# Optimization experiments

Hardware: AMD Instinct MI355X
Metric: run time of the kernel (lower is better)

Reference implementation:

```python
import jax, jax.numpy as jnp
import numpy as np
import math

NUM_HEADS = 16
HEAD_DIM = 64
EMBED = 1024
NUM_BUCKETS = 32
MAX_DISTANCE = 128


def _relative_position_bucket(relative_position, num_buckets=NUM_BUCKETS, max_distance=MAX_DISTANCE):
    # bidirectional T5 bucketing
    nb = num_buckets // 2
    relative_buckets = (relative_position > 0).astype(jnp.int32) * nb
    rp = jnp.abs(relative_position)
    max_exact = nb // 2
    is_small = rp < max_exact
    rp_safe = jnp.maximum(rp, 1)  # avoid log(0); masked by is_small anyway
    rp_large = max_exact + (
        jnp.log(rp_safe.astype(jnp.float32) / max_exact)
        / math.log(max_distance / max_exact)
        * (nb - max_exact)
    ).astype(jnp.int32)
    rp_large = jnp.minimum(rp_large, nb - 1)
    return relative_buckets + jnp.where(is_small, rp, rp_large)


def compute_bias(rel_emb, q_len, k_len):
    ctx = jnp.arange(q_len)[:, None]
    mem = jnp.arange(k_len)[None, :]
    buckets = _relative_position_bucket(mem - ctx)  # [q,k]
    values = rel_emb[buckets]                       # [q,k,H]
    return jnp.transpose(values, (2, 0, 1))[None]   # [1,H,q,k]


def setup_inputs() -> dict:
    key = jax.random.key(0)
    ks = jax.random.split(key, 6)
    std = 0.02
    B, S = 2, 2048
    inner = NUM_HEADS * HEAD_DIM
    return {
        "input_ids": jax.random.normal(ks[0], (B, S, EMBED), dtype=jnp.float32),
        "Wq": jax.random.normal(ks[1], (EMBED, inner), dtype=jnp.float32) * std,
        "Wk": jax.random.normal(ks[2], (EMBED, inner), dtype=jnp.float32) * std,
        "Wv": jax.random.normal(ks[3], (EMBED, inner), dtype=jnp.float32) * std,
        "Wo": jax.random.normal(ks[4], (inner, EMBED), dtype=jnp.float32) * std,
        "rel_emb": jax.random.normal(ks[5], (NUM_BUCKETS, NUM_HEADS), dtype=jnp.float32) * std,
    }


def reference(input_ids, Wq, Wk, Wv, Wo, rel_emb):
    B, S, _ = input_ids.shape
    H, D = NUM_HEADS, HEAD_DIM
    q = (input_ids @ Wq).reshape(B, S, H, D).transpose(0, 2, 1, 3)  # [B,H,S,D]
    k = (input_ids @ Wk).reshape(B, S, H, D).transpose(0, 2, 1, 3)
    v = (input_ids @ Wv).reshape(B, S, H, D).transpose(0, 2, 1, 3)
    scores = jnp.einsum("bhqd,bhkd->bhqk", q, k)  # no 1/sqrt(d) scaling (T5 style)
    position_bias = compute_bias(rel_emb, S, S)   # [1,H,S,S]
    scores = scores + position_bias
    attn = jax.nn.softmax(scores, axis=-1)
    out = jnp.einsum("bhqk,bhkd->bhqd", attn, v)
    out = out.transpose(0, 2, 1, 3).reshape(B, S, H * D)
    out = out @ Wo
    return out, position_bias
```

## Files before the change

### kernel.cpp

```cpp
#include <hip/hip_runtime.h>
#include <stdint.h>

#define S_LEN 2048
#define NH 16
#define EMB 1024
#define L2E 1.44269504f

typedef __attribute__((ext_vector_type(8))) short bf16x8;
typedef __attribute__((ext_vector_type(4))) float floatx4;
typedef const __attribute__((address_space(1))) unsigned int* gas_u32p;
typedef __attribute__((address_space(3))) unsigned int* las_u32p;

static __device__ __forceinline__ void gld_lds16(const void* g, void* l) {
  __builtin_amdgcn_global_load_lds((gas_u32p)g, (las_u32p)l, 16, 0, 0);
}

static __device__ __forceinline__ unsigned short f2bf(float f) {
  unsigned int u = __float_as_uint(f);
  unsigned int r = (u + 0x7FFFu + ((u >> 16) & 1u)) >> 16;
  return (unsigned short)r;
}
static __device__ __forceinline__ unsigned short f2bf_fast(float f) {
  return (unsigned short)((__float_as_uint(f) + 0x8000u) >> 16);
}

static __device__ __forceinline__ void bias_block(int bb, int tid,
                                                  const float* __restrict__ lut,
                                                  float* __restrict__ bias_out) {
#pragma unroll 4
  for (int e = 0; e < 256; e++) {
    int i = (bb << 16) + (e << 8) + tid;
    int h = i >> 20;
    int rem = i & 1048575;
    int q = rem >> 9;
    int k4 = (rem & 511) << 2;
    const float* lr = lut + h * 4096 + (k4 - q + 2048);
    floatx4 v = (floatx4){lr[0], lr[1], lr[2], lr[3]};
    __builtin_nontemporal_store(v, (floatx4*)&bias_out[(size_t)i * 4]);
  }
}

__global__ __launch_bounds__(256) void prep_kernel(const float* __restrict__ X,
                                                   const float* __restrict__ Wq,
                                                   const float* __restrict__ Wk,
                                                   const float* __restrict__ Wv,
                                                   const float* __restrict__ Wo,
                                                   const float* __restrict__ rel,
                                                   unsigned short* __restrict__ Xb,
                                                   unsigned short* __restrict__ WT,
                                                   float* __restrict__ lut) {
  __shared__ float tile[32][33];
  const int bid = blockIdx.x, tid = threadIdx.x;
  if (bid < 4096) {
    int i = bid * 256 + tid;
    float4 v = ((const float4*)X)[i];
    ushort4 o;
    o.x = f2bf(v.x); o.y = f2bf(v.y); o.z = f2bf(v.z); o.w = f2bf(v.w);
    ((ushort4*)Xb)[i] = o;
  } else if (bid < 8192) {
    int w = (bid - 4096) >> 10, t = (bid - 4096) & 1023;
    const float* in = (w == 0) ? Wq : (w == 1) ? Wk : (w == 2) ? Wv : Wo;
    unsigned short* o = WT + (size_t)w * 1048576;
    int bx = t & 31, by = t >> 5;
    int tx = tid & 31, ty = tid >> 5;
    int x = bx * 32 + tx, y0 = by * 32 + ty;
#pragma unroll
    for (int j = 0; j < 4; j++)
      tile[ty + 8 * j][tx] = in[(y0 + 8 * j) * EMB + x];
    __syncthreads();
    int x2 = by * 32 + tx, y2 = bx * 32 + ty;
#pragma unroll
    for (int j = 0; j < 4; j++)
      o[(y2 + 8 * j) * EMB + x2] = f2bf(tile[tx][ty + 8 * j]);
  } else {
    int idx = (bid - 8192) * 256 + tid;
    int delta = idx - 2048;
    int bucket = (delta > 0) ? 16 : 0;
    int rp = (delta < 0) ? -delta : delta;
    int bl;
    if (rp < 8) bl = rp;
    else bl = 8 + (rp >= 12) + (rp >= 16) + (rp >= 23) + (rp >= 32) + (rp >= 46) + (rp >= 64) + (rp >= 91);
    bucket += bl;
#pragma unroll
    for (int h = 0; h < NH; h++)
      lut[h * 4096 + idx] = rel[bucket * NH + h];
  }
}

__global__ __launch_bounds__(256) void gemm_qkv(const unsigned short* __restrict__ A,
                                                const unsigned short* __restrict__ BT,
                                                unsigned short* __restrict__ oQ,
                                                unsigned short* __restrict__ oK,
                                                unsigned short* __restrict__ oV,
                                                const float* __restrict__ lut,
                                                float* __restrict__ bias_out) {
  __shared__ __align__(16) unsigned short As[128 * 64];
  __shared__ __align__(16) unsigned short Bs[128 * 64];
  const int tid = threadIdx.x;
  const int id = blockIdx.x;
  if (id >= 768) {
    bias_block(id - 768, tid, lut, bias_out);
    return;
  }
  const int wave = tid >> 6, lane = tid & 63;
  const int quad = lane >> 4, lm = lane & 15;
  const int wm = wave & 1, wn = wave >> 1;
  const int mBase = (id / 24) * 128, nBase = (id % 24) * 128;
  const int gg = (lane & 7) ^ (lane >> 3);
  const int srow = lane >> 3;
  floatx4 acc[4][4];
#pragma unroll
  for (int i = 0; i < 4; i++)
#pragma unroll
    for (int j = 0; j < 4; j++) acc[i][j] = (floatx4){0.f, 0.f, 0.f, 0.f};

  for (int kt = 0; kt < 16; kt++) {
    int k0 = kt * 64;
    __syncthreads();
#pragma unroll
    for (int c = 0; c < 4; c++) {
      int chunk = wave * 4 + c;
      int row = chunk * 8 + srow;
      gld_lds16(&A[(size_t)(mBase + row) * 1024 + k0 + gg * 8], &As[chunk * 512]);
      gld_lds16(&BT[(size_t)(nBase + row) * 1024 + k0 + gg * 8], &Bs[chunk * 512]);
    }
    __syncthreads();
#pragma unroll
    for (int hh = 0; hh < 2; hh++) {
      bf16x8 af[4], bfr[4];
#pragma unroll
      for (int i = 0; i < 4; i++)
        af[i] = *(const bf16x8*)&As[(wm * 64 + i * 16 + lm) * 64 + (((hh << 2) + quad) ^ (lm & 7)) * 8];
#pragma unroll
      for (int j = 0; j < 4; j++)
        bfr[j] = *(const bf16x8*)&Bs[(wn * 64 + j * 16 + lm) * 64 + (((hh << 2) + quad) ^ (lm & 7)) * 8];
#pragma unroll
      for (int i = 0; i < 4; i++)
#pragma unroll
        for (int j = 0; j < 4; j++)
          acc[i][j] = __builtin_amdgcn_mfma_f32_16x16x32_bf16(af[i], bfr[j], acc[i][j], 0, 0, 0);
    }
  }
  const int which = nBase >> 10;
  if (which == 2) {
#pragma unroll
    for (int i = 0; i < 4; i++)
#pragma unroll
      for (int j = 0; j < 4; j++) {
        int hd = (nBase - 2048) + wn * 64 + j * 16 + lm;
        int h = hd >> 6, d = hd & 63;
        int m = mBase + wm * 64 + i * 16 + quad * 4;
        int b = m >> 11, s = m & 2047;
        union { unsigned short u[4]; uint2 v; } pk;
#pragma unroll
        for (int r = 0; r < 4; r++) pk.u[r] = f2bf(acc[i][j][r]);
        *(uint2*)&oV[(((size_t)(b * NH + h) * 64 + d) * S_LEN) + s] = pk.v;
      }
  } else {
#pragma unroll
    for (int i = 0; i < 4; i++)
#pragma unroll
      for (int j = 0; j < 4; j++)
#pragma unroll
        for (int r = 0; r < 4; r++) {
          int row = mBase + wm * 64 + i * 16 + quad * 4 + r;
          int col = nBase + wn * 64 + j * 16 + lm;
          int b = row >> 11, s = row & 2047;
          int cw = col & 1023;
          int h = cw >> 6, d = cw & 63;
          float v = acc[i][j][r];
          if (which == 0) v *= L2E;
          unsigned short sv = f2bf(v);
          if (which == 0) oQ[(((size_t)(b * NH + h) * S_LEN + s) * 64) + d] = sv;
          else            oK[(((size_t)(b * NH + h) * S_LEN + s) * 64) + d] = sv;
        }
  }
}

__global__ __launch_bounds__(256) void gemm_out(const unsigned short* __restrict__ A,
                                                const unsigned short* __restrict__ BT,
                                                float* __restrict__ oF,
                                                const float* __restrict__ lut,
                                                float* __restrict__ bias_out) {
  __shared__ __align__(16) unsigned short As[128 * 64];
  __shared__ __align__(16) unsigned short Bs[128 * 64];
  const int tid = threadIdx.x;
  const int id = blockIdx.x;
  if (id >= 256) {
    bias_block(160 + (id - 256), tid, lut, bias_out);
    return;
  }
  const int wave = tid >> 6, lane = tid & 63;
  const int quad = lane >> 4, lm = lane & 15;
  const int wm = wave & 1, wn = wave >> 1;
  const int mBase = (id >> 3) * 128, nBase = (id & 7) * 128;
  const int gg = (lane & 7) ^ (lane >> 3);
  const int srow = lane >> 3;
  floatx4 acc[4][4];
#pragma unroll
  for (int i = 0; i < 4; i++)
#pragma unroll
    for (int j = 0; j < 4; j++) acc[i][j] = (floatx4){0.f, 0.f, 0.f, 0.f};

  for (int kt = 0; kt < 16; kt++) {
    int k0 = kt * 64;
    __syncthreads();
#pragma unroll
    for (int c = 0; c < 4; c++) {
      int chunk = wave * 4 + c;
      int row = chunk * 8 + srow;
      gld_lds16(&A[(size_t)(mBase + row) * 1024 + k0 + gg * 8], &As[chunk * 512]);
      gld_lds16(&BT[(size_t)(nBase + row) * 1024 + k0 + gg * 8], &Bs[chunk * 512]);
    }
    __syncthreads();
#pragma unroll
    for (int hh = 0; hh < 2; hh++) {
      bf16x8 af[4], bfr[4];
#pragma unroll
      for (int i = 0; i < 4; i++)
        af[i] = *(const bf16x8*)&As[(wm * 64 + i * 16 + lm) * 64 + (((hh << 2) + quad) ^ (lm & 7)) * 8];
#pragma unroll
      for (int j = 0; j < 4; j++)
        bfr[j] = *(const bf16x8*)&Bs[(wn * 64 + j * 16 + lm) * 64 + (((hh << 2) + quad) ^ (lm & 7)) * 8];
#pragma unroll
      for (int i = 0; i < 4; i++)
#pragma unroll
        for (int j = 0; j < 4; j++)
          acc[i][j] = __builtin_amdgcn_mfma_f32_16x16x32_bf16(af[i], bfr[j], acc[i][j], 0, 0, 0);
    }
  }
#pragma unroll
  for (int i = 0; i < 4; i++)
#pragma unroll
    for (int j = 0; j < 4; j++)
#pragma unroll
      for (int r = 0; r < 4; r++) {
        int row = mBase + wm * 64 + i * 16 + quad * 4 + r;
        int col = nBase + wn * 64 + j * 16 + lm;
        oF[(size_t)row * 1024 + col] = acc[i][j][r];
      }
}

__global__ __launch_bounds__(512, 4) void attn_kernel(const unsigned short* __restrict__ Qb,
                                                      const unsigned short* __restrict__ Kb,
                                                      const unsigned short* __restrict__ Vtb,
                                                      const float* __restrict__ lut,
                                                      unsigned short* __restrict__ Ob) {
  __shared__ __align__(16) unsigned short Kl[2][2][2048];
  __shared__ __align__(16) unsigned short Vl[2][2][2048];
  __shared__ float lutS[512];
  const int tid = threadIdx.x;
  const int wave = tid >> 6, lane = tid & 63;
  const int quad = lane >> 4, lm = lane & 15;
  const int ws = wave & 3, half = wave >> 2;
  const int ii = blockIdx.x;
  const int bh = (ii & 7) * 4 + ((ii >> 3) & 3);
  const int qTile = (ii >> 5) * 128;
  const int b = bh >> 4, h = bh & 15;
  const unsigned short* Qp = Qb + (size_t)bh * S_LEN * 64;
  const unsigned short* Kp = Kb + (size_t)bh * S_LEN * 64;
  const unsigned short* Vp = Vtb + (size_t)bh * 64 * S_LEN;
  const float* lrow = lut + h * 4096;
  const float cneg = lrow[0] * L2E, cpos = lrow[4095] * L2E;
  const int srow = lane >> 3;
  const int gg = (lane & 7) ^ (srow & 7);
  const int vrow = lane >> 2;
  const int vgg = (lane & 3) ^ ((lane >> 3) & 3);
  const int qw = qTile + ws * 32;
  const int lmP = (lm & 3) | ((lm & 4) << 1) | ((lm & 8) >> 1);
  const int qq4 = ((quad & 1) << 3) | ((quad & 2) << 1);

  lutS[tid & 511] = lrow[2048 - 256 + (tid & 511)] * L2E;

  bf16x8 aq[2][2];
#pragma unroll
  for (int g = 0; g < 2; g++)
#pragma unroll
    for (int hh = 0; hh < 2; hh++)
      aq[g][hh] = *(const bf16x8*)&Qp[(qw + g * 16 + lm) * 64 + hh * 32 + quad * 8];

  floatx4 accO[2][4];
#pragma unroll
  for (int g = 0; g < 2; g++)
#pragma unroll
    for (int d = 0; d < 4; d++) accO[g][d] = (floatx4){0.f, 0.f, 0.f, 0.f};
  float lp[2] = {0.f, 0.f};

  const int vswz = ((lm >> 1) & 3);

  {
    const int kBase = half << 10;
    gld_lds16(&Kp[(size_t)(kBase + ws * 8 + srow) * 64 + gg * 8], &Kl[half][0][ws * 512]);
    gld_lds16(&Vp[(size_t)(ws * 16 + vrow) * S_LEN + kBase + vgg * 8], &Vl[half][0][ws * 512]);
  }

  for (int ktl = 0; ktl < 32; ktl++) {
    const int buf = ktl & 1;
    const int kBase = (half << 10) + ktl * 32;
    __syncthreads();
    if (ktl < 31) {
      const int kn = kBase + 32;
      gld_lds16(&Kp[(size_t)(kn + ws * 8 + srow) * 64 + gg * 8], &Kl[half][buf ^ 1][ws * 512]);
      gld_lds16(&Vp[(size_t)(ws * 16 + vrow) * S_LEN + kn + vgg * 8], &Vl[half][buf ^ 1][ws * 512]);
    }
    const unsigned short* Kbuf = Kl[half][buf];
    const unsigned short* Vbuf = Vl[half][buf];

    const bool farTile = (kBase + 122 <= qTile) || (kBase >= qTile + 218);
    const float cfar = (kBase < qTile) ? cneg : cpos;

    floatx4 s4[2][2];
    __builtin_amdgcn_s_setprio(1);
#pragma unroll
    for (int nt = 0; nt < 2; nt++) {
      int rbase = (nt * 16 + lmP) * 64;
      bf16x8 kf0 = *(const bf16x8*)&Kbuf[rbase + ((quad ^ (lmP & 7)) << 3)];
      bf16x8 kf1 = *(const bf16x8*)&Kbuf[rbase + (((4 + quad) ^ (lmP & 7)) << 3)];
#pragma unroll
      for (int g = 0; g < 2; g++) {
        floatx4 z = (floatx4){0.f, 0.f, 0.f, 0.f};
        z = __builtin_amdgcn_mfma_f32_16x16x32_bf16(kf0, aq[g][0], z, 0, 0, 0);
        z = __builtin_amdgcn_mfma_f32_16x16x32_bf16(kf1, aq[g][1], z, 0, 0, 0);
        s4[g][nt] = z;
      }
    }
    __builtin_amdgcn_s_setprio(0);

    bf16x8 pa[2];
#pragma unroll
    for (int g = 0; g < 2; g++) {
      const int b0 = kBase + qq4 - (qw + g * 16 + lm) + 256;
      float psum = 0.f;
      unsigned w00, w01, w10, w11;
#pragma unroll
      for (int nt = 0; nt < 2; nt++) {
        float sv0, sv1, sv2, sv3;
        if (farTile) {
          sv0 = s4[g][nt][0] + cfar; sv1 = s4[g][nt][1] + cfar;
          sv2 = s4[g][nt][2] + cfar; sv3 = s4[g][nt][3] + cfar;
        } else {
          const float* lb = &lutS[b0 + nt * 16];
          sv0 = s4[g][nt][0] + lb[0]; sv1 = s4[g][nt][1] + lb[1];
          sv2 = s4[g][nt][2] + lb[2]; sv3 = s4[g][nt][3] + lb[3];
        }
        float p0 = __builtin_amdgcn_exp2f(sv0);
        float p1 = __builtin_amdgcn_exp2f(sv1);
        float p2 = __builtin_amdgcn_exp2f(sv2);
        float p3 = __builtin_amdgcn_exp2f(sv3);
        psum += (p0 + p1) + (p2 + p3);
        unsigned wlo, whi;
        asm("v_cvt_pk_bf16_f32 %0, %1, %2" : "=v"(wlo) : "v"(p0), "v"(p1));
        asm("v_cvt_pk_bf16_f32 %0, %1, %2" : "=v"(whi) : "v"(p2), "v"(p3));
        if (nt == 0) { w00 = wlo; w01 = whi; } else { w10 = wlo; w11 = whi; }
      }
      lp[g] += psum;
      asm("v_permlane32_swap_b32 %0, %1" : "+v"(w00), "+v"(w10));
      asm("v_permlane32_swap_b32 %0, %1" : "+v"(w01), "+v"(w11));
      union { unsigned u[4]; bf16x8 v; } pk;
      pk.u[0] = w00; pk.u[1] = w01; pk.u[2] = w10; pk.u[3] = w11;
      pa[g] = pk.v;
    }

    __builtin_amdgcn_s_setprio(1);
#pragma unroll
    for (int d = 0; d < 4; d++) {
      bf16x8 vf = *(const bf16x8*)&Vbuf[(d * 16 + lm) * 32 + ((quad ^ vswz) << 3)];
      accO[0][d] = __builtin_amdgcn_mfma_f32_16x16x32_bf16(pa[0], vf, accO[0][d], 0, 0, 0);
      accO[1][d] = __builtin_amdgcn_mfma_f32_16x16x32_bf16(pa[1], vf, accO[1][d], 0, 0, 0);
    }
    __builtin_amdgcn_s_setprio(0);
  }

#pragma unroll
  for (int g = 0; g < 2; g++) {
    lp[g] += __shfl_xor(lp[g], 16, 64);
    lp[g] += __shfl_xor(lp[g], 32, 64);
  }

  __syncthreads();
  float* Ox = (ws < 2) ? ((float*)&Kl[0][0][0]) + ws * 2048 : ((float*)&Vl[0][0][0]) + (ws - 2) * 2048;
  float* lpf = lutS;
  if (half == 1) {
#pragma unroll
    for (int g = 0; g < 2; g++) {
#pragma unroll
      for (int d = 0; d < 4; d++)
#pragma unroll
        for (int r = 0; r < 4; r++)
          Ox[(g * 16 + quad * 4 + r) * 64 + d * 16 + lm] = accO[g][d][r];
      if (quad == 0) lpf[ws * 32 + g * 16 + lm] = lp[g];
    }
  }
  __syncthreads();
  if (half == 0) {
    float ltot[2];
#pragma unroll
    for (int g = 0; g < 2; g++) ltot[g] = lp[g] + lpf[ws * 32 + g * 16 + lm];
#pragma unroll
    for (int g = 0; g < 2; g++) {
      float linv[4];
#pragma unroll
      for (int r = 0; r < 4; r++) linv[r] = 1.f / __shfl(ltot[g], quad * 4 + r, 64);
#pragma unroll
      for (int d = 0; d < 4; d++)
#pragma unroll
        for (int r = 0; r < 4; r++) {
          float val = accO[g][d][r] + Ox[(g * 16 + quad * 4 + r) * 64 + d * 16 + lm];
          int q = qw + g * 16 + quad * 4 + r;
          int col = h * 64 + d * 16 + lm;
          Ob[((size_t)(b * S_LEN + q)) * 1024 + col] = f2bf_fast(val * linv[r]);
        }
    }
  }
}

extern "C" void kernel_launch(void* const* d_in, const int* in_sizes, int n_in,
                              void* d_out, int out_size, void* d_ws, size_t ws_size,
                              hipStream_t stream) {
  const float* X   = (const float*)d_in[0];
  const float* Wq  = (const float*)d_in[1];
  const float* Wk  = (const float*)d_in[2];
  const float* Wv  = (const float*)d_in[3];
  const float* Wo  = (const float*)d_in[4];
  const float* rel = (const float*)d_in[5];
  float* out = (float*)d_out;
  float* bias_out = out + 4194304;

  char* ws = (char*)d_ws;
  unsigned short* Xb  = (unsigned short*)(ws);
  unsigned short* WT  = (unsigned short*)(ws + (size_t)(8u << 20));
  unsigned short* Qb  = (unsigned short*)(ws + (size_t)(16u << 20));
  unsigned short* Kb  = (unsigned short*)(ws + (size_t)(24u << 20));
  unsigned short* Vtb = (unsigned short*)(ws + (size_t)(32u << 20));
  unsigned short* Ob  = (unsigned short*)(ws + (size_t)(40u << 20));
  float* lut          = (float*)(ws + (size_t)(48u << 20));

  prep_kernel<<<8208, 256, 0, stream>>>(X, Wq, Wk, Wv, Wo, rel, Xb, WT, lut);
  gemm_qkv<<<928, 256, 0, stream>>>(Xb, WT, Qb, Kb, Vtb, lut, bias_out);
  attn_kernel<<<512, 512, 0, stream>>>(Qb, Kb, Vtb, lut, Ob);
  gemm_out<<<352, 256, 0, stream>>>(Ob, WT + 3 * 1048576, out, lut, bias_out);
}
```

Measured before the change: 401.1 us.

## Process two K/V tiles per barrier and remap GEMM block order across XCDs

The attention loop now stages two 32-key K/V tiles per iteration into a 4-deep LDS ring, so there is one __syncthreads per 64 keys instead of per 32 and more prefetch runs ahead. LDS per block for K/V doubles, which could lower occupancy under launch_bounds(512,4). Both GEMM kernels also permute block IDs so that consecutive tiles land on the same XCD (id&7 striding), aiming for better L2 reuse of A and B rows.

```diff
diff --git a/kernel.cpp b/kernel.cpp
--- a/kernel.cpp
+++ b/kernel.cpp
@@ -105,7 +105,8 @@
   const int wave = tid >> 6, lane = tid & 63;
   const int quad = lane >> 4, lm = lane & 15;
   const int wm = wave & 1, wn = wave >> 1;
-  const int mBase = (id / 24) * 128, nBase = (id % 24) * 128;
+  const int id2 = (id & 7) * 96 + (id >> 3);
+  const int mBase = (id2 / 24) * 128, nBase = (id2 % 24) * 128;
   const int gg = (lane & 7) ^ (lane >> 3);
   const int srow = lane >> 3;
   floatx4 acc[4][4];
@@ -193,7 +194,8 @@
   const int wave = tid >> 6, lane = tid & 63;
   const int quad = lane >> 4, lm = lane & 15;
   const int wm = wave & 1, wn = wave >> 1;
-  const int mBase = (id >> 3) * 128, nBase = (id & 7) * 128;
+  const int id2 = (id & 7) * 32 + (id >> 3);
+  const int mBase = (id2 >> 3) * 128, nBase = (id2 & 7) * 128;
   const int gg = (lane & 7) ^ (lane >> 3);
   const int srow = lane >> 3;
   floatx4 acc[4][4];
@@ -246,8 +248,8 @@
                                                       const unsigned short* __restrict__ Vtb,
                                                       const float* __restrict__ lut,
                                                       unsigned short* __restrict__ Ob) {
-  __shared__ __align__(16) unsigned short Kl[2][2][2048];
-  __shared__ __align__(16) unsigned short Vl[2][2][2048];
+  __shared__ __align__(16) unsigned short Kl[2][4][2048];
+  __shared__ __align__(16) unsigned short Vl[2][4][2048];
   __shared__ float lutS[512];
   const int tid = threadIdx.x;
   const int wave = tid >> 6, lane = tid & 63;
@@ -289,86 +291,95 @@
   const int vswz = ((lm >> 1) & 3);
 
   {
-    const int kBase = half << 10;
-    gld_lds16(&Kp[(size_t)(kBase + ws * 8 + srow) * 64 + gg * 8], &Kl[half][0][ws * 512]);
-    gld_lds16(&Vp[(size_t)(ws * 16 + vrow) * S_LEN + kBase + vgg * 8], &Vl[half][0][ws * 512]);
-  }
-
-  for (int ktl = 0; ktl < 32; ktl++) {
-    const int buf = ktl & 1;
-    const int kBase = (half << 10) + ktl * 32;
-    __syncthreads();
-    if (ktl < 31) {
-      const int kn = kBase + 32;
-      gld_lds16(&Kp[(size_t)(kn + ws * 8 + srow) * 64 + gg * 8], &Kl[half][buf ^ 1][ws * 512]);
-      gld_lds16(&Vp[(size_t)(ws * 16 + vrow) * S_LEN + kn + vgg * 8], &Vl[half][buf ^ 1][ws * 512]);
-    }
-    const unsigned short* Kbuf = Kl[half][buf];
-    const unsigned short* Vbuf = Vl[half][buf];
-
-    const bool farTile = (kBase + 122 <= qTile) || (kBase >= qTile + 218);
-    const float cfar = (kBase < qTile) ? cneg : cpos;
-
-    floatx4 s4[2][2];
-    __builtin_amdgcn_s_setprio(1);
-#pragma unroll
-    for (int nt = 0; nt < 2; nt++) {
-      int rbase = (nt * 16 + lmP) * 64;
-      bf16x8 kf0 = *(const bf16x8*)&Kbuf[rbase + ((quad ^ (lmP & 7)) << 3)];
-      bf16x8 kf1 = *(const bf16x8*)&Kbuf[rbase + (((4 + quad) ^ (lmP & 7)) << 3)];
+    const int kb0 = half << 10;
+    gld_lds16(&Kp[(size_t)(kb0 + ws * 8 + srow) * 64 + gg * 8], &Kl[half][0][ws * 512]);
+    gld_lds16(&Vp[(size_t)(ws * 16 + vrow) * S_LEN + kb0 + vgg * 8], &Vl[half][0][ws * 512]);
+    gld_lds16(&Kp[(size_t)(kb0 + 32 + ws * 8 + srow) * 64 + gg * 8], &Kl[half][1][ws * 512]);
+    gld_lds16(&Vp[(size_t)(ws * 16 + vrow) * S_LEN + kb0 + 32 + vgg * 8], &Vl[half][1][ws * 512]);
+  }
+
+  for (int p = 0; p < 16; p++) {
+    __syncthreads();
+    if (p < 15) {
+      const int kn = (half << 10) + p * 64 + 64;
+      const int b2 = (2 * p + 2) & 3, b3 = (2 * p + 3) & 3;
+      gld_lds16(&Kp[(size_t)(kn + ws * 8 + srow) * 64 + gg * 8], &Kl[half][b2][ws * 512]);
+      gld_lds16(&Vp[(size_t)(ws * 16 + vrow) * S_LEN + kn + vgg * 8], &Vl[half][b2][ws * 512]);
+      gld_lds16(&Kp[(size_t)(kn + 32 + ws * 8 + srow) * 64 + gg * 8], &Kl[half][b3][ws * 512]);
+      gld_lds16(&Vp[(size_t)(ws * 16 + vrow) * S_LEN + kn + 32 + vgg * 8], &Vl[half][b3][ws * 512]);
+    }
+#pragma unroll
+    for (int u = 0; u < 2; u++) {
+      const int ktl = 2 * p + u;
+      const int buf = ktl & 3;
+      const int kBase = (half << 10) + ktl * 32;
+      const unsigned short* Kbuf = Kl[half][buf];
+      const unsigned short* Vbuf = Vl[half][buf];
+
+      const bool farTile = (kBase + 122 <= qTile) || (kBase >= qTile + 218);
+      const float cfar = (kBase < qTile) ? cneg : cpos;
+
+      floatx4 s4[2][2];
+      __builtin_amdgcn_s_setprio(1);
+#pragma unroll
+      for (int nt = 0; nt < 2; nt++) {
+        int rbase = (nt * 16 + lmP) * 64;
+        bf16x8 kf0 = *(const bf16x8*)&Kbuf[rbase + ((quad ^ (lmP & 7)) << 3)];
+        bf16x8 kf1 = *(const bf16x8*)&Kbuf[rbase + (((4 + quad) ^ (lmP & 7)) << 3)];
+#pragma unroll
+        for (int g = 0; g < 2; g++) {
+          floatx4 z = (floatx4){0.f, 0.f, 0.f, 0.f};
+          z = __builtin_amdgcn_mfma_f32_16x16x32_bf16(kf0, aq[g][0], z, 0, 0, 0);
+          z = __builtin_amdgcn_mfma_f32_16x16x32_bf16(kf1, aq[g][1], z, 0, 0, 0);
+          s4[g][nt] = z;
+        }
+      }
+      __builtin_amdgcn_s_setprio(0);
+
+      bf16x8 pa[2];
 #pragma unroll
       for (int g = 0; g < 2; g++) {
-        floatx4 z = (floatx4){0.f, 0.f, 0.f, 0.f};
-        z = __builtin_amdgcn_mfma_f32_16x16x32_bf16(kf0, aq[g][0], z, 0, 0, 0);
-        z = __builtin_amdgcn_mfma_f32_16x16x32_bf16(kf1, aq[g][1], z, 0, 0, 0);
-        s4[g][nt] = z;
+        const int b0 = kBase + qq4 - (qw + g * 16 + lm) + 256;
+        float psum = 0.f;
+        unsigned w00, w01, w10, w11;
+#pragma unroll
+        for (int nt = 0; nt < 2; nt++) {
+          float sv0, sv1, sv2, sv3;
+          if (farTile) {
+            sv0 = s4[g][nt][0] + cfar; sv1 = s4[g][nt][1] + cfar;
+            sv2 = s4[g][nt][2] + cfar; sv3 = s4[g][nt][3] + cfar;
+          } else {
+            const float* lb = &lutS[b0 + nt * 16];
+            sv0 = s4[g][nt][0] + lb[0]; sv1 = s4[g][nt][1] + lb[1];
+            sv2 = s4[g][nt][2] + lb[2]; sv3 = s4[g][nt][3] + lb[3];
+          }
+          float p0 = __builtin_amdgcn_exp2f(sv0);
+          float p1 = __builtin_amdgcn_exp2f(sv1);
+          float p2 = __builtin_amdgcn_exp2f(sv2);
+          float p3 = __builtin_amdgcn_exp2f(sv3);
+          psum += (p0 + p1) + (p2 + p3);
+          unsigned wlo, whi;
+          asm("v_cvt_pk_bf16_f32 %0, %1, %2" : "=v"(wlo) : "v"(p0), "v"(p1));
+          asm("v_cvt_pk_bf16_f32 %0, %1, %2" : "=v"(whi) : "v"(p2), "v"(p3));
+          if (nt == 0) { w00 = wlo; w01 = whi; } else { w10 = wlo; w11 = whi; }
+        }
+        lp[g] += psum;
+        asm("v_permlane32_swap_b32 %0, %1" : "+v"(w00), "+v"(w10));
+        asm("v_permlane32_swap_b32 %0, %1" : "+v"(w01), "+v"(w11));
+        union { unsigned u[4]; bf16x8 v; } pk;
+        pk.u[0] = w00; pk.u[1] = w01; pk.u[2] = w10; pk.u[3] = w11;
+        pa[g] = pk.v;
       }
-    }
-    __builtin_amdgcn_s_setprio(0);
-
-    bf16x8 pa[2];
-#pragma unroll
-    for (int g = 0; g < 2; g++) {
-      const int b0 = kBase + qq4 - (qw + g * 16 + lm) + 256;
-      float psum = 0.f;
-      unsigned w00, w01, w10, w11;
-#pragma unroll
-      for (int nt = 0; nt < 2; nt++) {
-        float sv0, sv1, sv2, sv3;
-        if (farTile) {
-          sv0 = s4[g][nt][0] + cfar; sv1 = s4[g][nt][1] + cfar;
-          sv2 = s4[g][nt][2] + cfar; sv3 = s4[g][nt][3] + cfar;
-        } else {
-          const float* lb = &lutS[b0 + nt * 16];
-          sv0 = s4[g][nt][0] + lb[0]; sv1 = s4[g][nt][1] + lb[1];
-          sv2 = s4[g][nt][2] + lb[2]; sv3 = s4[g][nt][3] + lb[3];
-        }
-        float p0 = __builtin_amdgcn_exp2f(sv0);
-        float p1 = __builtin_amdgcn_exp2f(sv1);
-        float p2 = __builtin_amdgcn_exp2f(sv2);
-        float p3 = __builtin_amdgcn_exp2f(sv3);
-        psum += (p0 + p1) + (p2 + p3);
-        unsigned wlo, whi;
-        asm("v_cvt_pk_bf16_f32 %0, %1, %2" : "=v"(wlo) : "v"(p0), "v"(p1));
-        asm("v_cvt_pk_bf16_f32 %0, %1, %2" : "=v"(whi) : "v"(p2), "v"(p3));
-        if (nt == 0) { w00 = wlo; w01 = whi; } else { w10 = wlo; w11 = whi; }
+
+      __builtin_amdgcn_s_setprio(1);
+#pragma unroll
+      for (int d = 0; d < 4; d++) {
+        bf16x8 vf = *(const bf16x8*)&Vbuf[(d * 16 + lm) * 32 + ((quad ^ vswz) << 3)];
+        accO[0][d] = __builtin_amdgcn_mfma_f32_16x16x32_bf16(pa[0], vf, accO[0][d], 0, 0, 0);
+        accO[1][d] = __builtin_amdgcn_mfma_f32_16x16x32_bf16(pa[1], vf, accO[1][d], 0, 0, 0);
       }
-      lp[g] += psum;
-      asm("v_permlane32_swap_b32 %0, %1" : "+v"(w00), "+v"(w10));
-      asm("v_permlane32_swap_b32 %0, %1" : "+v"(w01), "+v"(w11));
-      union { unsigned u[4]; bf16x8 v; } pk;
-      pk.u[0] = w00; pk.u[1] = w01; pk.u[2] = w10; pk.u[3] = w11;
-      pa[g] = pk.v;
-    }
-
-    __builtin_amdgcn_s_setprio(1);
-#pragma unroll
-    for (int d = 0; d < 4; d++) {
-      bf16x8 vf = *(const bf16x8*)&Vbuf[(d * 16 + lm) * 32 + ((quad ^ vswz) << 3)];
-      accO[0][d] = __builtin_amdgcn_mfma_f32_16x16x32_bf16(pa[0], vf, accO[0][d], 0, 0, 0);
-      accO[1][d] = __builtin_amdgcn_mfma_f32_16x16x32_bf16(pa[1], vf, accO[1][d], 0, 0, 0);
-    }
-    __builtin_amdgcn_s_setprio(0);
+      __builtin_amdgcn_s_setprio(0);
+    }
   }
 
 #pragma unroll
```

Result: no change. 406.0 us (+1.2%).

## Load K/V fragments directly from global memory and swizzle GEMM block order

Applied to the files above, without the earlier changes.

The attention kernel drops the LDS double-buffered K/V staging and per-iteration barriers. Each wave now loads its K and V MFMA fragments straight from global memory (relying on L1/L2), which removes the LDS traffic and sync points. The cost is that the four waves sharing a half now reload the same K/V tiles redundantly and global-load latency is exposed without explicit prefetch. Separately, both GEMM kernels remap block IDs with an XCD-aware interleave so neighbouring tiles share L2 on the same die.

```diff
diff --git a/kernel.cpp b/kernel.cpp
--- a/kernel.cpp
+++ b/kernel.cpp
@@ -105,7 +105,8 @@
   const int wave = tid >> 6, lane = tid & 63;
   const int quad = lane >> 4, lm = lane & 15;
   const int wm = wave & 1, wn = wave >> 1;
-  const int mBase = (id / 24) * 128, nBase = (id % 24) * 128;
+  const int id2 = (id & 7) * 96 + (id >> 3);
+  const int mBase = (id2 / 24) * 128, nBase = (id2 % 24) * 128;
   const int gg = (lane & 7) ^ (lane >> 3);
   const int srow = lane >> 3;
   floatx4 acc[4][4];
@@ -193,7 +194,8 @@
   const int wave = tid >> 6, lane = tid & 63;
   const int quad = lane >> 4, lm = lane & 15;
   const int wm = wave & 1, wn = wave >> 1;
-  const int mBase = (id >> 3) * 128, nBase = (id & 7) * 128;
+  const int id2 = (id & 7) * 32 + (id >> 3);
+  const int mBase = (id2 >> 3) * 128, nBase = (id2 & 7) * 128;
   const int gg = (lane & 7) ^ (lane >> 3);
   const int srow = lane >> 3;
   floatx4 acc[4][4];
@@ -246,8 +248,7 @@
                                                       const unsigned short* __restrict__ Vtb,
                                                       const float* __restrict__ lut,
                                                       unsigned short* __restrict__ Ob) {
-  __shared__ __align__(16) unsigned short Kl[2][2][2048];
-  __shared__ __align__(16) unsigned short Vl[2][2][2048];
+  __shared__ float OxS[4][2048];
   __shared__ float lutS[512];
   const int tid = threadIdx.x;
   const int wave = tid >> 6, lane = tid & 63;
@@ -262,16 +263,15 @@
   const unsigned short* Vp = Vtb + (size_t)bh * 64 * S_LEN;
   const float* lrow = lut + h * 4096;
   const float cneg = lrow[0] * L2E, cpos = lrow[4095] * L2E;
-  const int srow = lane >> 3;
-  const int gg = (lane & 7) ^ (srow & 7);
-  const int vrow = lane >> 2;
-  const int vgg = (lane & 3) ^ ((lane >> 3) & 3);
   const int qw = qTile + ws * 32;
   const int lmP = (lm & 3) | ((lm & 4) << 1) | ((lm & 8) >> 1);
   const int qq4 = ((quad & 1) << 3) | ((quad & 2) << 1);
 
   lutS[tid & 511] = lrow[2048 - 256 + (tid & 511)] * L2E;
 
+  const unsigned short* kA = Kp + lmP * 64 + quad * 8;
+  const unsigned short* vA = Vp + lm * S_LEN + quad * 8;
+
   bf16x8 aq[2][2];
 #pragma unroll
   for (int g = 0; g < 2; g++)
@@ -286,25 +286,19 @@
     for (int d = 0; d < 4; d++) accO[g][d] = (floatx4){0.f, 0.f, 0.f, 0.f};
   float lp[2] = {0.f, 0.f};
 
-  const int vswz = ((lm >> 1) & 3);
-
-  {
-    const int kBase = half << 10;
-    gld_lds16(&Kp[(size_t)(kBase + ws * 8 + srow) * 64 + gg * 8], &Kl[half][0][ws * 512]);
-    gld_lds16(&Vp[(size_t)(ws * 16 + vrow) * S_LEN + kBase + vgg * 8], &Vl[half][0][ws * 512]);
-  }
+  __syncthreads();
 
   for (int ktl = 0; ktl < 32; ktl++) {
-    const int buf = ktl & 1;
     const int kBase = (half << 10) + ktl * 32;
-    __syncthreads();
-    if (ktl < 31) {
-      const int kn = kBase + 32;
-      gld_lds16(&Kp[(size_t)(kn + ws * 8 + srow) * 64 + gg * 8], &Kl[half][buf ^ 1][ws * 512]);
-      gld_lds16(&Vp[(size_t)(ws * 16 + vrow) * S_LEN + kn + vgg * 8], &Vl[half][buf ^ 1][ws * 512]);
-    }
-    const unsigned short* Kbuf = Kl[half][buf];
-    const unsigned short* Vbuf = Vl[half][buf];
+
+    bf16x8 kf00 = *(const bf16x8*)&kA[(size_t)kBase * 64];
+    bf16x8 kf01 = *(const bf16x8*)&kA[(size_t)kBase * 64 + 32];
+    bf16x8 kf10 = *(const bf16x8*)&kA[(size_t)(kBase + 16) * 64];
+    bf16x8 kf11 = *(const bf16x8*)&kA[(size_t)(kBase + 16) * 64 + 32];
+    bf16x8 vf0 = *(const bf16x8*)&vA[kBase];
+    bf16x8 vf1 = *(const bf16x8*)&vA[16 * S_LEN + kBase];
+    bf16x8 vf2 = *(const bf16x8*)&vA[32 * S_LEN + kBase];
+    bf16x8 vf3 = *(const bf16x8*)&vA[48 * S_LEN + kBase];
 
     const bool farTile = (kBase + 122 <= qTile) || (kBase >= qTile + 218);
     const float cfar = (kBase < qTile) ? cneg : cpos;
@@ -312,17 +306,15 @@
     floatx4 s4[2][2];
     __builtin_amdgcn_s_setprio(1);
 #pragma unroll
-    for (int nt = 0; nt < 2; nt++) {
-      int rbase = (nt * 16 + lmP) * 64;
-      bf16x8 kf0 = *(const bf16x8*)&Kbuf[rbase + ((quad ^ (lmP & 7)) << 3)];
-      bf16x8 kf1 = *(const bf16x8*)&Kbuf[rbase + (((4 + quad) ^ (lmP & 7)) << 3)];
-#pragma unroll
-      for (int g = 0; g < 2; g++) {
-        floatx4 z = (floatx4){0.f, 0.f, 0.f, 0.f};
-        z = __builtin_amdgcn_mfma_f32_16x16x32_bf16(kf0, aq[g][0], z, 0, 0, 0);
-        z = __builtin_amdgcn_mfma_f32_16x16x32_bf16(kf1, aq[g][1], z, 0, 0, 0);
-        s4[g][nt] = z;
-      }
+    for (int g = 0; g < 2; g++) {
+      floatx4 z = (floatx4){0.f, 0.f, 0.f, 0.f};
+      z = __builtin_amdgcn_mfma_f32_16x16x32_bf16(kf00, aq[g][0], z, 0, 0, 0);
+      z = __builtin_amdgcn_mfma_f32_16x16x32_bf16(kf01, aq[g][1], z, 0, 0, 0);
+      s4[g][0] = z;
+      floatx4 z2 = (floatx4){0.f, 0.f, 0.f, 0.f};
+      z2 = __builtin_amdgcn_mfma_f32_16x16x32_bf16(kf10, aq[g][0], z2, 0, 0, 0);
+      z2 = __builtin_amdgcn_mfma_f32_16x16x32_bf16(kf11, aq[g][1], z2, 0, 0, 0);
+      s4[g][1] = z2;
     }
     __builtin_amdgcn_s_setprio(0);
 
@@ -362,12 +354,14 @@
     }
 
     __builtin_amdgcn_s_setprio(1);
-#pragma unroll
-    for (int d = 0; d < 4; d++) {
-      bf16x8 vf = *(const bf16x8*)&Vbuf[(d * 16 + lm) * 32 + ((quad ^ vswz) << 3)];
-      accO[0][d] = __builtin_amdgcn_mfma_f32_16x16x32_bf16(pa[0], vf, accO[0][d], 0, 0, 0);
-      accO[1][d] = __builtin_amdgcn_mfma_f32_16x16x32_bf16(pa[1], vf, accO[1][d], 0, 0, 0);
-    }
+    accO[0][0] = __builtin_amdgcn_mfma_f32_16x16x32_bf16(pa[0], vf0, accO[0][0], 0, 0, 0);
+    accO[1][0] = __builtin_amdgcn_mfma_f32_16x16x32_bf16(pa[1], vf0, accO[1][0], 0, 0, 0);
+    accO[0][1] = __builtin_amdgcn_mfma_f32_16x16x32_bf16(pa[0], vf1, accO[0][1], 0, 0, 0);
+    accO[1][1] = __builtin_amdgcn_mfma_f32_16x16x32_bf16(pa[1], vf1, accO[1][1], 0, 0, 0);
+    accO[0][2] = __builtin_amdgcn_mfma_f32_16x16x32_bf16(pa[0], vf2, accO[0][2], 0, 0, 0);
+    accO[1][2] = __builtin_amdgcn_mfma_f32_16x16x32_bf16(pa[1], vf2, accO[1][2], 0, 0, 0);
+    accO[0][3] = __builtin_amdgcn_mfma_f32_16x16x32_bf16(pa[0], vf3, accO[0][3], 0, 0, 0);
+    accO[1][3] = __builtin_amdgcn_mfma_f32_16x16x32_bf16(pa[1], vf3, accO[1][3], 0, 0, 0);
     __builtin_amdgcn_s_setprio(0);
   }
 
@@ -378,7 +372,7 @@
   }
 
   __syncthreads();
-  float* Ox = (ws < 2) ? ((float*)&Kl[0][0][0]) + ws * 2048 : ((float*)&Vl[0][0][0]) + (ws - 2) * 2048;
+  float* Ox = &OxS[ws][0];
   float* lpf = lutS;
   if (half == 1) {
 #pragma unroll
```

Result: slower. 474.0 us (+18.2%).

## Interleave position-bias writes into attention loop and swizzle GEMM block order

Applied to the files above, without the earlier changes.

Moves the 256 MB position-bias output stores from extra blocks appended to the QKV and output GEMMs into the attention kernel's key-tile loop. Each attention block now writes a slice of the bias per iteration, so the store traffic can overlap with the compute-bound MFMA work. It also remaps block IDs in both GEMMs so consecutive blocks spread across tiles, likely to improve cache locality across XCDs. The risk is that the extra memory traffic and registers inside the attention loop slow down its inner pipeline.

```diff
diff --git a/kernel.cpp b/kernel.cpp
--- a/kernel.cpp
+++ b/kernel.cpp
@@ -22,22 +22,6 @@
 }
 static __device__ __forceinline__ unsigned short f2bf_fast(float f) {
   return (unsigned short)((__float_as_uint(f) + 0x8000u) >> 16);
-}
-
-static __device__ __forceinline__ void bias_block(int bb, int tid,
-                                                  const float* __restrict__ lut,
-                                                  float* __restrict__ bias_out) {
-#pragma unroll 4
-  for (int e = 0; e < 256; e++) {
-    int i = (bb << 16) + (e << 8) + tid;
-    int h = i >> 20;
-    int rem = i & 1048575;
-    int q = rem >> 9;
-    int k4 = (rem & 511) << 2;
-    const float* lr = lut + h * 4096 + (k4 - q + 2048);
-    floatx4 v = (floatx4){lr[0], lr[1], lr[2], lr[3]};
-    __builtin_nontemporal_store(v, (floatx4*)&bias_out[(size_t)i * 4]);
-  }
 }
 
 __global__ __launch_bounds__(256) void prep_kernel(const float* __restrict__ X,
@@ -91,21 +75,16 @@
                                                 const unsigned short* __restrict__ BT,
                                                 unsigned short* __restrict__ oQ,
                                                 unsigned short* __restrict__ oK,
-                                                unsigned short* __restrict__ oV,
-                                                const float* __restrict__ lut,
-                                                float* __restrict__ bias_out) {
+                                                unsigned short* __restrict__ oV) {
   __shared__ __align__(16) unsigned short As[128 * 64];
   __shared__ __align__(16) unsigned short Bs[128 * 64];
   const int tid = threadIdx.x;
   const int id = blockIdx.x;
-  if (id >= 768) {
-    bias_block(id - 768, tid, lut, bias_out);
-    return;
-  }
   const int wave = tid >> 6, lane = tid & 63;
   const int quad = lane >> 4, lm = lane & 15;
   const int wm = wave & 1, wn = wave >> 1;
-  const int mBase = (id / 24) * 128, nBase = (id % 24) * 128;
+  const int id2 = (id & 7) * 96 + (id >> 3);
+  const int mBase = (id2 / 24) * 128, nBase = (id2 % 24) * 128;
   const int gg = (lane & 7) ^ (lane >> 3);
   const int srow = lane >> 3;
   floatx4 acc[4][4];
@@ -179,21 +158,16 @@
 
 __global__ __launch_bounds__(256) void gemm_out(const unsigned short* __restrict__ A,
                                                 const unsigned short* __restrict__ BT,
-                                                float* __restrict__ oF,
-                                                const float* __restrict__ lut,
-                                                float* __restrict__ bias_out) {
+                                                float* __restrict__ oF) {
   __shared__ __align__(16) unsigned short As[128 * 64];
   __shared__ __align__(16) unsigned short Bs[128 * 64];
   const int tid = threadIdx.x;
   const int id = blockIdx.x;
-  if (id >= 256) {
-    bias_block(160 + (id - 256), tid, lut, bias_out);
-    return;
-  }
   const int wave = tid >> 6, lane = tid & 63;
   const int quad = lane >> 4, lm = lane & 15;
   const int wm = wave & 1, wn = wave >> 1;
-  const int mBase = (id >> 3) * 128, nBase = (id & 7) * 128;
+  const int id2 = (id & 7) * 32 + (id >> 3);
+  const int mBase = (id2 >> 3) * 128, nBase = (id2 & 7) * 128;
   const int gg = (lane & 7) ^ (lane >> 3);
   const int srow = lane >> 3;
   floatx4 acc[4][4];
@@ -245,7 +219,8 @@
                                                       const unsigned short* __restrict__ Kb,
                                                       const unsigned short* __restrict__ Vtb,
                                                       const float* __restrict__ lut,
-                                                      unsigned short* __restrict__ Ob) {
+                                                      unsigned short* __restrict__ Ob,
+                                                      float* __restrict__ bias_out) {
   __shared__ __align__(16) unsigned short Kl[2][2][2048];
   __shared__ __align__(16) unsigned short Vl[2][2][2048];
   __shared__ float lutS[512];
@@ -369,6 +344,19 @@
       accO[1][d] = __builtin_amdgcn_mfma_f32_16x16x32_bf16(pa[1], vf, accO[1][d], 0, 0, 0);
     }
     __builtin_amdgcn_s_setprio(0);
+
+#pragma unroll
+    for (int u = 0; u < 2; u++) {
+      int e = ktl * 2 + u;
+      int i = (ii << 15) + (e << 9) + tid;
+      int hb = i >> 20;
+      int rem = i & 1048575;
+      int q = rem >> 9;
+      int k4 = (rem & 511) << 2;
+      const float* lr = lut + hb * 4096 + (k4 - q + 2048);
+      floatx4 bv = (floatx4){lr[0], lr[1], lr[2], lr[3]};
+      __builtin_nontemporal_store(bv, (floatx4*)&bias_out[(size_t)i * 4]);
+    }
   }
 
 #pragma unroll
@@ -436,7 +424,7 @@
   float* lut          = (float*)(ws + (size_t)(48u << 20));
 
   prep_kernel<<<8208, 256, 0, stream>>>(X, Wq, Wk, Wv, Wo, rel, Xb, WT, lut);
-  gemm_qkv<<<928, 256, 0, stream>>>(Xb, WT, Qb, Kb, Vtb, lut, bias_out);
-  attn_kernel<<<512, 512, 0, stream>>>(Qb, Kb, Vtb, lut, Ob);
-  gemm_out<<<352, 256, 0, stream>>>(Ob, WT + 3 * 1048576, out, lut, bias_out);
-}
+  gemm_qkv<<<768, 256, 0, stream>>>(Xb, WT, Qb, Kb, Vtb);
+  attn_kernel<<<512, 512, 0, stream>>>(Qb, Kb, Vtb, lut, Ob, bias_out);
+  gemm_out<<<256, 256, 0, stream>>>(Ob, WT + 3 * 1048576, out);
+}
```

Result: faster. 386.5 us (median of 2 runs) (-3.6%).
